# Performance work log

Hardware: AMD Instinct MI355X
Metric: run time of the kernel (lower is better)

Reference implementation:

```python
import jax, jax.numpy as jnp
import numpy as np

B, T, F, CI, CO, K, DIL = 16, 512, 32, 128, 128, 3, 2


def setup_inputs() -> dict:
    key = jax.random.key(0)
    k1, k2, k3 = jax.random.split(key, 3)
    x = jax.random.normal(k1, (B, T, F, CI), dtype=jnp.float32)
    # torch Conv1d weight per feature: [CO, CI, K]; stack over features -> [F, CO, CI, K]
    fan_in = CI * K
    bound = 1.0 / np.sqrt(fan_in)
    w = jax.random.uniform(k2, (F, CO, CI, K), dtype=jnp.float32, minval=-bound, maxval=bound)
    b = jax.random.uniform(k3, (F, CO), dtype=jnp.float32, minval=-bound, maxval=bound)
    return {"x": x, "w": w, "b": b}


def reference(x, w, b):
    # Causal dilated conv, independent filters per feature.
    left_pad = DIL * (K - 1)
    xpad = jnp.pad(x, ((0, 0), (left_pad, 0), (0, 0), (0, 0)))  # [B, T+L, F, CI]
    # taps[k] = xpad[:, k*DIL : k*DIL + T] -> stack over kernel taps: [K, B, T, F, CI]
    taps = jnp.stack([xpad[:, k * DIL:k * DIL + T] for k in range(K)], axis=0)
    # y[b,t,f,o] = sum_{k,i} taps[k,b,t,f,i] * w[f,o,i,k] + b[f,o]
    y = jnp.einsum('kbtfi,foik->btfo', taps, w) + b[None, None, :, :]
    return y  # dropout p=0.0 (eval) is identity
```

## Files before the change

kernel.cpp:

```cpp
#include <hip/hip_runtime.h>
#include <stdint.h>

#define B_ 16
#define T_ 512
#define F_ 32
#define CI_ 128
#define CO_ 128
#define K_ 3
#define LPAD 4
#define TM 64
#define XROWS (TM + LPAD)
#define XPITCH 136
#define WPITCH 32
#define CHUNK_ELEMS (CO_ * WPITCH)
#define NCHUNK 12
#define NXV 5

typedef __attribute__((ext_vector_type(8))) __bf16 bf16x8;
typedef __attribute__((ext_vector_type(4))) float f32x4;

__device__ __forceinline__ uint16_t f2bf(float x) {
  uint32_t u = __builtin_bit_cast(uint32_t, x);
  u += 0x7fffu + ((u >> 16) & 1u);
  return (uint16_t)(u >> 16);
}

__global__ __launch_bounds__(256) void repack_w(const float* __restrict__ w,
                                                uint16_t* __restrict__ wt2) {
  int idx = blockIdx.x * 256 + threadIdx.x;
  int i = idx & (CI_ - 1);
  int fo = idx >> 7;
  int o = fo & (CO_ - 1);
  int f = fo >> 7;
  const float* src = w + (size_t)idx * K_;
  float a0 = src[0], a1 = src[1], a2 = src[2];
  size_t base = ((size_t)f * NCHUNK + (i >> 5)) * CHUNK_ELEMS + o * WPITCH + (i & 31);
  wt2[base] = f2bf(a0);
  wt2[base + 4 * (size_t)CHUNK_ELEMS] = f2bf(a1);
  wt2[base + 8 * (size_t)CHUNK_ELEMS] = f2bf(a2);
}

template <bool PACKED>
__global__ __launch_bounds__(512, 4) void conv_main(
    const float* __restrict__ x, const uint16_t* __restrict__ wt2,
    const float* __restrict__ wraw, const float* __restrict__ bias,
    float* __restrict__ y) {
  __shared__ __align__(16) uint16_t xs[2][XROWS * XPITCH];

  const int bid = blockIdx.x;

  if (((bid >> 8) ^ bid) & 1) {
    __builtin_amdgcn_s_sleep(127);
    __builtin_amdgcn_s_sleep(127);
  }

  const int f = bid >> 4;
  const int b = bid & 15;

  const int tid = threadIdx.x;
  const int lane = tid & 63;
  const int wave = tid >> 6;
  const int l15 = lane & 15;
  const int quad = lane >> 4;
  const int co0 = wave * 16;

  bf16x8 wreg[NCHUNK];
  if constexpr (PACKED) {
    const uint16_t* wp = wt2 + (size_t)f * NCHUNK * CHUNK_ELEMS + (co0 + l15) * WPITCH + quad * 8;
#pragma unroll
    for (int c = 0; c < NCHUNK; ++c)
      wreg[c] = *(const bf16x8*)(wp + c * CHUNK_ELEMS);
  } else {
#pragma unroll
    for (int c = 0; c < NCHUNK; ++c) {
      int tap = c >> 2, i0 = (c & 3) * 32 + quad * 8;
      const float* ws = wraw + (((size_t)(f * CO_ + co0 + l15)) * CI_ + i0) * K_ + tap;
      union { bf16x8 v; uint16_t h[8]; } u;
#pragma unroll
      for (int j = 0; j < 8; ++j) u.h[j] = f2bf(ws[j * K_]);
      wreg[c] = u.v;
    }
  }
  const float4 bb = *(const float4*)(bias + f * CO_ + co0 + quad * 4);

  const float* xb = x + ((size_t)b * T_ * F_ + f) * CI_;
  float4 xr[NXV];

  auto load_x = [&](int t0) {
#pragma unroll
    for (int it = 0; it < NXV; ++it) {
      int idx = tid + it * 512;
      if (idx < XROWS * 32) {
        int row = idx >> 5, c4 = idx & 31;
        int t = t0 - LPAD + row;
        xr[it] = (t >= 0) ? *(const float4*)(xb + (size_t)t * (F_ * CI_) + c4 * 4)
                          : make_float4(0.f, 0.f, 0.f, 0.f);
      }
    }
  };
  auto store_x = [&](uint16_t* dst) {
#pragma unroll
    for (int it = 0; it < NXV; ++it) {
      int idx = tid + it * 512;
      if (idx < XROWS * 32) {
        int row = idx >> 5, c4 = idx & 31;
        uint2 pk;
        pk.x = (uint32_t)f2bf(xr[it].x) | ((uint32_t)f2bf(xr[it].y) << 16);
        pk.y = (uint32_t)f2bf(xr[it].z) | ((uint32_t)f2bf(xr[it].w) << 16);
        *(uint2*)&dst[row * XPITCH + c4 * 4] = pk;
      }
    }
  };

  load_x(0);
  store_x(xs[0]);
  load_x(TM);
  __syncthreads();

  const int abase = l15 * XPITCH + quad * 8;

#pragma unroll 1
  for (int j = 0; j < 8; ++j) {
    const int t0 = j * TM;
    const uint16_t* xbuf = xs[j & 1];

    f32x4 acc[4];
#pragma unroll
    for (int fm = 0; fm < 4; ++fm) acc[fm] = (f32x4){bb.x, bb.y, bb.z, bb.w};

#pragma unroll
    for (int c = 0; c < NCHUNK; ++c) {
      const int tap = c >> 2, ks = c & 3;
#pragma unroll
      for (int fm = 0; fm < 4; ++fm) {
        bf16x8 av = *(const bf16x8*)&xbuf[abase + (2 * tap + fm * 16) * XPITCH + ks * 32];
        acc[fm] = __builtin_amdgcn_mfma_f32_16x16x32_bf16(wreg[c], av, acc[fm], 0, 0, 0);
      }
    }

    float* yb = y + (((size_t)b * T_ + t0 + l15) * F_ + f) * CO_ + co0 + quad * 4;
#pragma unroll
    for (int fm = 0; fm < 4; ++fm) {
      *(float4*)(yb + (size_t)(fm * 16) * (F_ * CO_)) =
          make_float4(acc[fm][0], acc[fm][1], acc[fm][2], acc[fm][3]);
    }

    if (j < 7) {
      store_x(xs[(j + 1) & 1]);
      if (j < 6) load_x((j + 2) * TM);
      asm volatile("s_waitcnt lgkmcnt(0)" ::: "memory");
      __builtin_amdgcn_s_barrier();
    }
  }
}

extern "C" void kernel_launch(void* const* d_in, const int* in_sizes, int n_in,
                              void* d_out, int out_size, void* d_ws, size_t ws_size,
                              hipStream_t stream) {
  const float* x = (const float*)d_in[0];
  const float* w = (const float*)d_in[1];
  const float* bias = (const float*)d_in[2];
  float* y = (float*)d_out;

  const size_t wt2_bytes = (size_t)F_ * NCHUNK * CHUNK_ELEMS * sizeof(uint16_t);
  const int main_blocks = F_ * B_;

  if (ws_size >= wt2_bytes) {
    uint16_t* wt2 = (uint16_t*)d_ws;
    const int total = F_ * CO_ * CI_;
    repack_w<<<total / 256, 256, 0, stream>>>(w, wt2);
    conv_main<true><<<main_blocks, 512, 0, stream>>>(x, wt2, w, bias, y);
  } else {
    conv_main<false><<<main_blocks, 512, 0, stream>>>(x, (const uint16_t*)nullptr, w, bias, y);
  }
}
```

Before: 256.8 us.

## Switch to 32x32x16 MFMA tiles with 4 waves per block

```diff
diff --git a/kernel.cpp b/kernel.cpp
--- a/kernel.cpp
+++ b/kernel.cpp
@@ -11,13 +11,12 @@
 #define TM 64
 #define XROWS (TM + LPAD)
 #define XPITCH 136
-#define WPITCH 32
-#define CHUNK_ELEMS (CO_ * WPITCH)
-#define NCHUNK 12
-#define NXV 5
+#define NWCH 24
+#define WCH_ELEMS (CO_ * 16)
+#define NXV 9
 
 typedef __attribute__((ext_vector_type(8))) __bf16 bf16x8;
-typedef __attribute__((ext_vector_type(4))) float f32x4;
+typedef __attribute__((ext_vector_type(16))) float f32x16;
 
 __device__ __forceinline__ uint16_t f2bf(float x) {
   uint32_t u = __builtin_bit_cast(uint32_t, x);
@@ -26,7 +25,7 @@
 }
 
 __global__ __launch_bounds__(256) void repack_w(const float* __restrict__ w,
-                                                uint16_t* __restrict__ wt2) {
+                                                uint16_t* __restrict__ wt3) {
   int idx = blockIdx.x * 256 + threadIdx.x;
   int i = idx & (CI_ - 1);
   int fo = idx >> 7;
@@ -34,15 +33,16 @@
   int f = fo >> 7;
   const float* src = w + (size_t)idx * K_;
   float a0 = src[0], a1 = src[1], a2 = src[2];
-  size_t base = ((size_t)f * NCHUNK + (i >> 5)) * CHUNK_ELEMS + o * WPITCH + (i & 31);
-  wt2[base] = f2bf(a0);
-  wt2[base + 4 * (size_t)CHUNK_ELEMS] = f2bf(a1);
-  wt2[base + 8 * (size_t)CHUNK_ELEMS] = f2bf(a2);
+  size_t base = ((size_t)(f * NWCH + (i >> 4)) * CO_ + o) * 16 + (i & 15);
+  const size_t tapstride = (size_t)8 * CO_ * 16;
+  wt3[base] = f2bf(a0);
+  wt3[base + tapstride] = f2bf(a1);
+  wt3[base + 2 * tapstride] = f2bf(a2);
 }
 
 template <bool PACKED>
-__global__ __launch_bounds__(512, 4) void conv_main(
-    const float* __restrict__ x, const uint16_t* __restrict__ wt2,
+__global__ __launch_bounds__(256, 2) void conv_main(
+    const float* __restrict__ x, const uint16_t* __restrict__ wt3,
     const float* __restrict__ wraw, const float* __restrict__ bias,
     float* __restrict__ y) {
   __shared__ __align__(16) uint16_t xs[2][XROWS * XPITCH];
@@ -59,29 +59,32 @@
 
   const int tid = threadIdx.x;
   const int lane = tid & 63;
-  const int wave = tid >> 6;
-  const int l15 = lane & 15;
-  const int quad = lane >> 4;
-  const int co0 = wave * 16;
+  const int wco = tid >> 6;
+  const int l31 = lane & 31;
+  const int h = lane >> 5;
+  const int co0 = wco * 32;
 
-  bf16x8 wreg[NCHUNK];
+  bf16x8 wreg[NWCH];
   if constexpr (PACKED) {
-    const uint16_t* wp = wt2 + (size_t)f * NCHUNK * CHUNK_ELEMS + (co0 + l15) * WPITCH + quad * 8;
+    const uint16_t* wp = wt3 + ((size_t)f * NWCH * CO_ + co0 + l31) * 16 + h * 8;
 #pragma unroll
-    for (int c = 0; c < NCHUNK; ++c)
-      wreg[c] = *(const bf16x8*)(wp + c * CHUNK_ELEMS);
+    for (int c = 0; c < NWCH; ++c)
+      wreg[c] = *(const bf16x8*)(wp + (size_t)c * WCH_ELEMS);
   } else {
 #pragma unroll
-    for (int c = 0; c < NCHUNK; ++c) {
-      int tap = c >> 2, i0 = (c & 3) * 32 + quad * 8;
-      const float* ws = wraw + (((size_t)(f * CO_ + co0 + l15)) * CI_ + i0) * K_ + tap;
-      union { bf16x8 v; uint16_t h[8]; } u;
+    for (int c = 0; c < NWCH; ++c) {
+      int tap = c >> 3, ci0 = (c & 7) * 16 + h * 8;
+      const float* ws = wraw + (((size_t)(f * CO_ + co0 + l31)) * CI_ + ci0) * K_ + tap;
+      union { bf16x8 v; uint16_t hh[8]; } u;
 #pragma unroll
-      for (int j = 0; j < 8; ++j) u.h[j] = f2bf(ws[j * K_]);
+      for (int j = 0; j < 8; ++j) u.hh[j] = f2bf(ws[j * K_]);
       wreg[c] = u.v;
     }
   }
-  const float4 bb = *(const float4*)(bias + f * CO_ + co0 + quad * 4);
+  float4 bb[4];
+#pragma unroll
+  for (int g = 0; g < 4; ++g)
+    bb[g] = *(const float4*)(bias + f * CO_ + co0 + 8 * g + 4 * h);
 
   const float* xb = x + ((size_t)b * T_ * F_ + f) * CI_;
   float4 xr[NXV];
@@ -89,7 +92,7 @@
   auto load_x = [&](int t0) {
 #pragma unroll
     for (int it = 0; it < NXV; ++it) {
-      int idx = tid + it * 512;
+      int idx = tid + it * 256;
       if (idx < XROWS * 32) {
         int row = idx >> 5, c4 = idx & 31;
         int t = t0 - LPAD + row;
@@ -101,7 +104,7 @@
   auto store_x = [&](uint16_t* dst) {
 #pragma unroll
     for (int it = 0; it < NXV; ++it) {
-      int idx = tid + it * 512;
+      int idx = tid + it * 256;
       if (idx < XROWS * 32) {
         int row = idx >> 5, c4 = idx & 31;
         uint2 pk;
@@ -117,32 +120,41 @@
   load_x(TM);
   __syncthreads();
 
-  const int abase = l15 * XPITCH + quad * 8;
+  const int abase = l31 * XPITCH + h * 8;
 
 #pragma unroll 1
   for (int j = 0; j < 8; ++j) {
     const int t0 = j * TM;
     const uint16_t* xbuf = xs[j & 1];
 
-    f32x4 acc[4];
+    f32x16 acc0, acc1;
 #pragma unroll
-    for (int fm = 0; fm < 4; ++fm) acc[fm] = (f32x4){bb.x, bb.y, bb.z, bb.w};
+    for (int g = 0; g < 4; ++g) {
+      acc0[4 * g + 0] = bb[g].x; acc0[4 * g + 1] = bb[g].y;
+      acc0[4 * g + 2] = bb[g].z; acc0[4 * g + 3] = bb[g].w;
+      acc1[4 * g + 0] = bb[g].x; acc1[4 * g + 1] = bb[g].y;
+      acc1[4 * g + 2] = bb[g].z; acc1[4 * g + 3] = bb[g].w;
+    }
 
 #pragma unroll
-    for (int c = 0; c < NCHUNK; ++c) {
-      const int tap = c >> 2, ks = c & 3;
-#pragma unroll
-      for (int fm = 0; fm < 4; ++fm) {
-        bf16x8 av = *(const bf16x8*)&xbuf[abase + (2 * tap + fm * 16) * XPITCH + ks * 32];
-        acc[fm] = __builtin_amdgcn_mfma_f32_16x16x32_bf16(wreg[c], av, acc[fm], 0, 0, 0);
-      }
+    for (int c = 0; c < NWCH; ++c) {
+      const int tap = c >> 3, kc = c & 7;
+      const int off = abase + 2 * tap * XPITCH + kc * 16;
+      bf16x8 av0 = *(const bf16x8*)&xbuf[off];
+      bf16x8 av1 = *(const bf16x8*)&xbuf[off + 32 * XPITCH];
+      acc0 = __builtin_amdgcn_mfma_f32_32x32x16_bf16(wreg[c], av0, acc0, 0, 0, 0);
+      acc1 = __builtin_amdgcn_mfma_f32_32x32x16_bf16(wreg[c], av1, acc1, 0, 0, 0);
     }
 
-    float* yb = y + (((size_t)b * T_ + t0 + l15) * F_ + f) * CO_ + co0 + quad * 4;
 #pragma unroll
-    for (int fm = 0; fm < 4; ++fm) {
-      *(float4*)(yb + (size_t)(fm * 16) * (F_ * CO_)) =
-          make_float4(acc[fm][0], acc[fm][1], acc[fm][2], acc[fm][3]);
+    for (int ts = 0; ts < 2; ++ts) {
+      float* yb = y + (((size_t)b * T_ + t0 + 32 * ts + l31) * F_ + f) * CO_ + co0 + 4 * h;
+      const f32x16& a = ts ? acc1 : acc0;
+#pragma unroll
+      for (int g = 0; g < 4; ++g) {
+        *(float4*)(yb + 8 * g) =
+            make_float4(a[4 * g + 0], a[4 * g + 1], a[4 * g + 2], a[4 * g + 3]);
+      }
     }
 
     if (j < 7) {
@@ -162,15 +174,15 @@
   const float* bias = (const float*)d_in[2];
   float* y = (float*)d_out;
 
-  const size_t wt2_bytes = (size_t)F_ * NCHUNK * CHUNK_ELEMS * sizeof(uint16_t);
+  const size_t wt3_bytes = (size_t)F_ * NWCH * WCH_ELEMS * sizeof(uint16_t);
   const int main_blocks = F_ * B_;
 
-  if (ws_size >= wt2_bytes) {
-    uint16_t* wt2 = (uint16_t*)d_ws;
+  if (ws_size >= wt3_bytes) {
+    uint16_t* wt3 = (uint16_t*)d_ws;
     const int total = F_ * CO_ * CI_;
-    repack_w<<<total / 256, 256, 0, stream>>>(w, wt2);
-    conv_main<true><<<main_blocks, 512, 0, stream>>>(x, wt2, w, bias, y);
+    repack_w<<<total / 256, 256, 0, stream>>>(w, wt3);
+    conv_main<true><<<main_blocks, 256, 0, stream>>>(x, wt3, w, bias, y);
   } else {
-    conv_main<false><<<main_blocks, 512, 0, stream>>>(x, (const uint16_t*)nullptr, w, bias, y);
+    conv_main<false><<<main_blocks, 256, 0, stream>>>(x, (const uint16_t*)nullptr, w, bias, y);
   }
 }
```

After: 260.7 us. About the same (+1.5%).
